# Kernel tuning notes

Hardware: AMD Instinct MI355X
Metric: run time of the kernel (lower is better)

## Reference

```python
import jax, jax.numpy as jnp
import numpy as np

NUM_EMBEDDINGS = 1024
EMBEDDING_DIM = 256
COMMITMENT_COST = 0.25


def setup_inputs() -> dict:
    key = jax.random.key(0)
    k1, k2 = jax.random.split(key)
    z_e = jax.random.normal(k1, (32, 256, 32, 32), dtype=jnp.float32)
    # nn.init.uniform_(weight, -1/K, 1/K)
    bound = 1.0 / NUM_EMBEDDINGS
    weight = jax.random.uniform(k2, (NUM_EMBEDDINGS, EMBEDDING_DIM), dtype=jnp.float32,
                                minval=-bound, maxval=bound)
    return {"z_e": z_e, "weight": weight}


def reference(z_e, weight):
    B, C, H, W = z_e.shape
    sg = jax.lax.stop_gradient
    # (B, H, W, C) -> (N, C)
    flat = jnp.transpose(z_e, (0, 2, 3, 1)).reshape(-1, C)
    # squared L2 distances to each codebook vector: (N, K)
    dist = (jnp.sum(flat * flat, axis=1, keepdims=True)
            - 2.0 * flat @ weight.T
            + jnp.sum(weight * weight, axis=1))
    indices = jnp.argmin(dist, axis=1)  # (N,)
    # codebook lookup (equivalent to one-hot @ weight)
    quantized = weight[indices].reshape(B, H, W, C)
    quantized = jnp.transpose(quantized, (0, 3, 1, 2))  # (B, C, H, W)
    e_latent = jnp.mean((sg(quantized) - z_e) ** 2)
    q_latent = jnp.mean((quantized - sg(z_e)) ** 2)
    loss = q_latent + COMMITMENT_COST * e_latent
    # straight-through estimator
    quantized_st = z_e + sg(quantized - z_e)
    # codebook usage perplexity: avg_probs = mean of one-hot encodings
    n = flat.shape[0]
    counts = jax.ops.segment_sum(jnp.ones((n,), dtype=z_e.dtype), indices,
                                 num_segments=NUM_EMBEDDINGS)
    avg_probs = counts / n
    perplexity = jnp.exp(-jnp.sum(avg_probs * jnp.log(avg_probs + 1e-10)))
    return (quantized_st, loss, perplexity)
```

## Files before the change

kernel.cpp:

```cpp
#include <hip/hip_runtime.h>
#include <float.h>
#include <math.h>
#include <stdint.h>


#define NB   32
#define NC   256
#define NHW  1024
#define NK   1024
#define NELEM (NB*NC*NHW)

typedef __attribute__((ext_vector_type(8))) short bf16x8;
typedef __attribute__((ext_vector_type(4))) float f32x4;

__device__ __forceinline__ unsigned short f2bf(float f) {
    unsigned u = __float_as_uint(f);
    u += 0x7FFFu + ((u >> 16) & 1u);
    return (unsigned short)(u >> 16);
}

__global__ __launch_bounds__(256) void vq_prep(const float* __restrict__ w,
                                               unsigned short* __restrict__ cb,
                                               float* __restrict__ wsq,
                                               unsigned int* __restrict__ counts,
                                               float* __restrict__ loss_sum) {
    __shared__ float swsq[4][16];
    const int t   = blockIdx.x;
    const int tid = threadIdx.x;
    float sq = 0.f;
#pragma unroll
    for (int rep = 0; rep < 2; ++rep) {
        const int p = tid + rep * 256;
        const int cc = p >> 6, l = p & 63;
        const int n = l & 15, quad = l >> 4;
        const float* src = w + (t * 16 + n) * NC + cc * 32 + quad * 8;
        const float4 f0 = *(const float4*)src;
        const float4 f1 = *(const float4*)(src + 4);
        union { unsigned short u[8]; uint4 v; } pk;
        pk.u[0] = f2bf(-2.f * f0.x); pk.u[1] = f2bf(-2.f * f0.y);
        pk.u[2] = f2bf(-2.f * f0.z); pk.u[3] = f2bf(-2.f * f0.w);
        pk.u[4] = f2bf(-2.f * f1.x); pk.u[5] = f2bf(-2.f * f1.y);
        pk.u[6] = f2bf(-2.f * f1.z); pk.u[7] = f2bf(-2.f * f1.w);
        *(uint4*)(cb + (size_t)t * 4096 + cc * 512 + l * 8) = pk.v;
        sq = fmaf(f0.x, f0.x, sq); sq = fmaf(f0.y, f0.y, sq);
        sq = fmaf(f0.z, f0.z, sq); sq = fmaf(f0.w, f0.w, sq);
        sq = fmaf(f1.x, f1.x, sq); sq = fmaf(f1.y, f1.y, sq);
        sq = fmaf(f1.z, f1.z, sq); sq = fmaf(f1.w, f1.w, sq);
    }
    sq += __shfl_xor(sq, 16, 64);
    sq += __shfl_xor(sq, 32, 64);
    const int wv = tid >> 6, lane = tid & 63;
    if (lane < 16) swsq[wv][lane] = sq;
    __syncthreads();
    if (tid < 16)
        wsq[t * 16 + tid] = swsq[0][tid] + swsq[1][tid] + swsq[2][tid] + swsq[3][tid];
    if (t == 0) {
        for (int i = tid; i < NK; i += 256) counts[i] = 0u;
        if (tid == 0) loss_sum[0] = 0.f;
    }
}

__global__ __launch_bounds__(256, 2) void vq_main3(const float* __restrict__ z,
                                                   const float* __restrict__ w,
                                                   const float* __restrict__ wsq,
                                                   const unsigned short* __restrict__ cb,
                                                   unsigned int* __restrict__ counts,
                                                   float* __restrict__ loss_sum,
                                                   float* __restrict__ out) {
    __shared__ float sval[4][64];
    __shared__ int   sidx[4][64];
    __shared__ int   fidx[64];
    __shared__ float lred[4];

    const int tid  = threadIdx.x;
    const int wv   = tid >> 6;
    const int lane = tid & 63;
    const int n    = lane & 15;
    const int quad = lane >> 4;
    const int bid  = blockIdx.x;
    const int b    = bid >> 4;
    const int hw0  = (bid & 15) << 6;

    const float* zb = z + (size_t)b * (NC * NHW);

    bf16x8 bfr[4][8];
#pragma unroll
    for (int nt = 0; nt < 4; ++nt) {
#pragma unroll
        for (int cc = 0; cc < 8; ++cc) {
            const float* zp = zb + (size_t)(cc * 32 + quad * 8) * NHW + hw0 + nt * 16 + n;
            union { unsigned short u[8]; bf16x8 v; } pk;
#pragma unroll
            for (int j = 0; j < 8; ++j) pk.u[j] = f2bf(zp[(size_t)j * NHW]);
            bfr[nt][cc] = pk.v;
        }
    }

    float bv[4] = {FLT_MAX, FLT_MAX, FLT_MAX, FLT_MAX};
    int   bi[4] = {0, 0, 0, 0};
    const unsigned short* ap0 = cb + (size_t)(wv * 16) * 4096 + lane * 8;

    for (int mt = 0; mt < 16; ++mt) {
        const int kt = wv * 256 + mt * 16;
        const unsigned short* ap = ap0 + (size_t)mt * 4096;
        const f32x4 w4 = *(const f32x4*)(wsq + kt + quad * 4);
        f32x4 acc[4];
#pragma unroll
        for (int nt = 0; nt < 4; ++nt) acc[nt] = w4;
#pragma unroll
        for (int cc = 0; cc < 8; ++cc) {
            const bf16x8 af = *(const bf16x8*)(ap + cc * 512);
            acc[0] = __builtin_amdgcn_mfma_f32_16x16x32_bf16(af, bfr[0][cc], acc[0], 0, 0, 0);
            acc[1] = __builtin_amdgcn_mfma_f32_16x16x32_bf16(af, bfr[1][cc], acc[1], 0, 0, 0);
            acc[2] = __builtin_amdgcn_mfma_f32_16x16x32_bf16(af, bfr[2][cc], acc[2], 0, 0, 0);
            acc[3] = __builtin_amdgcn_mfma_f32_16x16x32_bf16(af, bfr[3][cc], acc[3], 0, 0, 0);
        }
#pragma unroll
        for (int nt = 0; nt < 4; ++nt) {
#pragma unroll
            for (int r = 0; r < 4; ++r) {
                const float v = acc[nt][r];
                if (v < bv[nt]) { bv[nt] = v; bi[nt] = kt + quad * 4 + r; }
            }
        }
    }

#pragma unroll
    for (int nt = 0; nt < 4; ++nt) {
#pragma unroll
        for (int off = 16; off <= 32; off <<= 1) {
            const float ov = __shfl_xor(bv[nt], off, 64);
            const int   ok = __shfl_xor(bi[nt], off, 64);
            if (ov < bv[nt] || (ov == bv[nt] && ok < bi[nt])) { bv[nt] = ov; bi[nt] = ok; }
        }
    }
    if (lane < 16) {
#pragma unroll
        for (int nt = 0; nt < 4; ++nt) {
            sval[wv][nt * 16 + lane] = bv[nt];
            sidx[wv][nt * 16 + lane] = bi[nt];
        }
    }
    __syncthreads();

    if (tid < 64) {
        float bestv = sval[0][tid];
        int   besti = sidx[0][tid];
#pragma unroll
        for (int q = 1; q < 4; ++q) {
            const float v = sval[q][tid];
            const int   k = sidx[q][tid];
            if (v < bestv || (v == bestv && k < besti)) { bestv = v; besti = k; }
        }
        fidx[tid] = besti;
        atomicAdd(&counts[besti], 1u);
    }
    __syncthreads();

    float lsum = 0.f;
    const int hwl = tid & 63;
    const int cg  = tid >> 6;
    const int myk = fidx[hwl];
    const float* wr  = w + myk * NC;
    const float* zp2 = zb + hw0 + hwl;
    float*       op  = out + (size_t)b * (NC * NHW) + hw0 + hwl;
#pragma unroll 4
    for (int p = 0; p < 16; ++p) {
        const int c0 = cg * 64 + p * 4;
        const float4 q4 = *(const float4*)(wr + c0);
        const float qa[4] = {q4.x, q4.y, q4.z, q4.w};
#pragma unroll
        for (int u = 0; u < 4; ++u) {
            const int c = c0 + u;
            const float zv = zp2[(size_t)c * NHW];
            const float d = qa[u] - zv;
            lsum = fmaf(d, d, lsum);
            op[(size_t)c * NHW] = qa[u];
        }
    }
#pragma unroll
    for (int off = 32; off; off >>= 1) lsum += __shfl_down(lsum, off, 64);
    if (lane == 0) lred[wv] = lsum;
    __syncthreads();
    if (tid == 0)
        atomicAdd(loss_sum, lred[0] + lred[1] + lred[2] + lred[3]);
}

__global__ __launch_bounds__(256) void vq_final(const unsigned int* __restrict__ counts,
                                                const float* __restrict__ loss_sum,
                                                float* __restrict__ out) {
    __shared__ float red[4];
    const int tid = threadIdx.x;
    float s = 0.f;
#pragma unroll
    for (int p = 0; p < 4; ++p) {
        const float pr = (float)counts[tid + p * 256] * (1.f / 32768.f);
        s = fmaf(pr, logf(pr + 1e-10f), s);
    }
#pragma unroll
    for (int off = 32; off; off >>= 1) s += __shfl_down(s, off, 64);
    if ((tid & 63) == 0) red[tid >> 6] = s;
    __syncthreads();
    if (tid == 0) {
        const float tot = red[0] + red[1] + red[2] + red[3];
        out[NELEM]     = loss_sum[0] * (1.25f / (float)NELEM);
        out[NELEM + 1] = expf(-tot);
    }
}

extern "C" void kernel_launch(void* const* d_in, const int* in_sizes, int n_in,
                              void* d_out, int out_size, void* d_ws, size_t ws_size,
                              hipStream_t stream) {
    const float* z = (const float*)d_in[0];
    const float* w = (const float*)d_in[1];
    float* out = (float*)d_out;

    float*          wsq      = (float*)d_ws;
    unsigned int*   counts   = (unsigned int*)((char*)d_ws + 4096);
    float*          loss_sum = (float*)((char*)d_ws + 8192);
    unsigned short* cbfrag   = (unsigned short*)((char*)d_ws + 16384);

    vq_prep <<<64,  256, 0, stream>>>(w, cbfrag, wsq, counts, loss_sum);
    vq_main3<<<512, 256, 0, stream>>>(z, w, wsq, cbfrag, counts, loss_sum, out);
    vq_final<<<1,   256, 0, stream>>>(counts, loss_sum, out);
}
```

Baseline: 123.2 us.

## Fuse final reduction into main kernel via last-block counter; vectorize epilogue

Removes the separate finalization kernel launch. The last block to finish, found with an atomic done-counter after a threadfence, computes the perplexity and loss outputs. The gather and output epilogue is also re-mapped so each thread handles 4 consecutive spatial positions per channel, using float4 loads and stores of z and out, while the codebook values become scalar gathers. This saves a launch and its gap and widens memory accesses, at the cost of an atomic counter and strided codebook reads.

```diff
diff --git a/kernel.cpp b/kernel.cpp
--- a/kernel.cpp
+++ b/kernel.cpp
@@ -23,7 +23,8 @@
                                                unsigned short* __restrict__ cb,
                                                float* __restrict__ wsq,
                                                unsigned int* __restrict__ counts,
-                                               float* __restrict__ loss_sum) {
+                                               float* __restrict__ loss_sum,
+                                               unsigned int* __restrict__ done) {
     __shared__ float swsq[4][16];
     const int t   = blockIdx.x;
     const int tid = threadIdx.x;
@@ -56,21 +57,23 @@
         wsq[t * 16 + tid] = swsq[0][tid] + swsq[1][tid] + swsq[2][tid] + swsq[3][tid];
     if (t == 0) {
         for (int i = tid; i < NK; i += 256) counts[i] = 0u;
-        if (tid == 0) loss_sum[0] = 0.f;
-    }
-}
-
-__global__ __launch_bounds__(256, 2) void vq_main3(const float* __restrict__ z,
+        if (tid == 0) { loss_sum[0] = 0.f; done[0] = 0u; }
+    }
+}
+
+__global__ __launch_bounds__(256, 2) void vq_main6(const float* __restrict__ z,
                                                    const float* __restrict__ w,
                                                    const float* __restrict__ wsq,
                                                    const unsigned short* __restrict__ cb,
                                                    unsigned int* __restrict__ counts,
                                                    float* __restrict__ loss_sum,
+                                                   unsigned int* __restrict__ done,
                                                    float* __restrict__ out) {
     __shared__ float sval[4][64];
     __shared__ int   sidx[4][64];
     __shared__ int   fidx[64];
     __shared__ float lred[4];
+    __shared__ int   amlast;
 
     const int tid  = threadIdx.x;
     const int wv   = tid >> 6;
@@ -158,24 +161,29 @@
     __syncthreads();
 
     float lsum = 0.f;
-    const int hwl = tid & 63;
-    const int cg  = tid >> 6;
-    const int myk = fidx[hwl];
-    const float* wr  = w + myk * NC;
-    const float* zp2 = zb + hw0 + hwl;
-    float*       op  = out + (size_t)b * (NC * NHW) + hw0 + hwl;
+    {
+        const int l4 = (tid & 15) * 4;
+        const int cq = tid >> 4;
+        int k4[4];
+#pragma unroll
+        for (int u = 0; u < 4; ++u) k4[u] = fidx[l4 + u];
+        const float* zp2 = zb + hw0 + l4;
+        float*       op  = out + (size_t)b * (NC * NHW) + hw0 + l4;
 #pragma unroll 4
-    for (int p = 0; p < 16; ++p) {
-        const int c0 = cg * 64 + p * 4;
-        const float4 q4 = *(const float4*)(wr + c0);
-        const float qa[4] = {q4.x, q4.y, q4.z, q4.w};
-#pragma unroll
-        for (int u = 0; u < 4; ++u) {
-            const int c = c0 + u;
-            const float zv = zp2[(size_t)c * NHW];
-            const float d = qa[u] - zv;
-            lsum = fmaf(d, d, lsum);
-            op[(size_t)c * NHW] = qa[u];
+        for (int p = 0; p < 16; ++p) {
+            const int c = cq + p * 16;
+            const float4 zq = *(const float4*)(zp2 + (size_t)c * NHW);
+            float4 q;
+            q.x = w[k4[0] * NC + c];
+            q.y = w[k4[1] * NC + c];
+            q.z = w[k4[2] * NC + c];
+            q.w = w[k4[3] * NC + c];
+            float d;
+            d = q.x - zq.x; lsum = fmaf(d, d, lsum);
+            d = q.y - zq.y; lsum = fmaf(d, d, lsum);
+            d = q.z - zq.z; lsum = fmaf(d, d, lsum);
+            d = q.w - zq.w; lsum = fmaf(d, d, lsum);
+            *(float4*)(op + (size_t)c * NHW) = q;
         }
     }
 #pragma unroll
@@ -184,27 +192,31 @@
     __syncthreads();
     if (tid == 0)
         atomicAdd(loss_sum, lred[0] + lred[1] + lred[2] + lred[3]);
-}
-
-__global__ __launch_bounds__(256) void vq_final(const unsigned int* __restrict__ counts,
-                                                const float* __restrict__ loss_sum,
-                                                float* __restrict__ out) {
-    __shared__ float red[4];
-    const int tid = threadIdx.x;
-    float s = 0.f;
-#pragma unroll
-    for (int p = 0; p < 4; ++p) {
-        const float pr = (float)counts[tid + p * 256] * (1.f / 32768.f);
-        s = fmaf(pr, logf(pr + 1e-10f), s);
-    }
-#pragma unroll
-    for (int off = 32; off; off >>= 1) s += __shfl_down(s, off, 64);
-    if ((tid & 63) == 0) red[tid >> 6] = s;
-    __syncthreads();
+
     if (tid == 0) {
-        const float tot = red[0] + red[1] + red[2] + red[3];
-        out[NELEM]     = loss_sum[0] * (1.25f / (float)NELEM);
-        out[NELEM + 1] = expf(-tot);
+        __threadfence();
+        amlast = (atomicAdd(done, 1u) == (unsigned)(gridDim.x - 1)) ? 1 : 0;
+    }
+    __syncthreads();
+    if (amlast) {
+        float s = 0.f;
+#pragma unroll
+        for (int p = 0; p < 4; ++p) {
+            const unsigned cnt = atomicAdd(&counts[tid + p * 256], 0u);
+            const float pr = (float)cnt * (1.f / 32768.f);
+            s = fmaf(pr, logf(pr + 1e-10f), s);
+        }
+#pragma unroll
+        for (int off = 32; off; off >>= 1) s += __shfl_down(s, off, 64);
+        __syncthreads();
+        if (lane == 0) lred[wv] = s;
+        __syncthreads();
+        if (tid == 0) {
+            const float tot = lred[0] + lred[1] + lred[2] + lred[3];
+            const float lv  = atomicAdd(loss_sum, 0.f);
+            out[NELEM]     = lv * (1.25f / (float)NELEM);
+            out[NELEM + 1] = expf(-tot);
+        }
     }
 }
 
@@ -218,9 +230,9 @@
     float*          wsq      = (float*)d_ws;
     unsigned int*   counts   = (unsigned int*)((char*)d_ws + 4096);
     float*          loss_sum = (float*)((char*)d_ws + 8192);
+    unsigned int*   done     = (unsigned int*)((char*)d_ws + 8196);
     unsigned short* cbfrag   = (unsigned short*)((char*)d_ws + 16384);
 
-    vq_prep <<<64,  256, 0, stream>>>(w, cbfrag, wsq, counts, loss_sum);
-    vq_main3<<<512, 256, 0, stream>>>(z, w, wsq, cbfrag, counts, loss_sum, out);
-    vq_final<<<1,   256, 0, stream>>>(counts, loss_sum, out);
-}
+    vq_prep <<<64,  256, 0, stream>>>(w, cbfrag, wsq, counts, loss_sum, done);
+    vq_main6<<<512, 256, 0, stream>>>(z, w, wsq, cbfrag, counts, loss_sum, done, out);
+}
```

Measured after the change: 142.7 us. 15.8% more time.

## Split distance/argmin and gather-scatter into separate kernels via global index buffer

Applied to the files above, without the earlier changes.

The fused main kernel is split in two. One kernel does the MFMA distance and argmin and writes the winning indices to a global workspace buffer. A new scatter kernel with a different grid then reads 4 indices per thread, loads z with float4, gathers codebook values and writes the output with float4 stores. The aim is to let the memory-bound gather/scatter phase run with more parallelism and vectorized, coalesced access instead of serialized per-block tails. The cost is an extra launch, plus a round trip of the index buffer and a second read of z.

```diff
diff --git a/kernel.cpp b/kernel.cpp
--- a/kernel.cpp
+++ b/kernel.cpp
@@ -60,17 +60,13 @@
     }
 }
 
-__global__ __launch_bounds__(256, 2) void vq_main3(const float* __restrict__ z,
-                                                   const float* __restrict__ w,
-                                                   const float* __restrict__ wsq,
-                                                   const unsigned short* __restrict__ cb,
-                                                   unsigned int* __restrict__ counts,
-                                                   float* __restrict__ loss_sum,
-                                                   float* __restrict__ out) {
+__global__ __launch_bounds__(256, 2) void vq_dist(const float* __restrict__ z,
+                                                  const float* __restrict__ wsq,
+                                                  const unsigned short* __restrict__ cb,
+                                                  unsigned int* __restrict__ counts,
+                                                  int* __restrict__ gfidx) {
     __shared__ float sval[4][64];
     __shared__ int   sidx[4][64];
-    __shared__ int   fidx[64];
-    __shared__ float lred[4];
 
     const int tid  = threadIdx.x;
     const int wv   = tid >> 6;
@@ -152,34 +148,47 @@
             const int   k = sidx[q][tid];
             if (v < bestv || (v == bestv && k < besti)) { bestv = v; besti = k; }
         }
-        fidx[tid] = besti;
+        gfidx[b * NHW + hw0 + tid] = besti;
         atomicAdd(&counts[besti], 1u);
     }
-    __syncthreads();
+}
+
+__global__ __launch_bounds__(256, 4) void vq_scatter(const float* __restrict__ z,
+                                                     const float* __restrict__ w,
+                                                     const int* __restrict__ gfidx,
+                                                     float* __restrict__ loss_sum,
+                                                     float* __restrict__ out) {
+    __shared__ float lred[4];
+    const int tid = threadIdx.x;
+    const int bid = blockIdx.x;
+    const int b   = bid >> 5;
+    const int c0  = (bid & 31) << 3;
+    const int hw4 = tid << 2;
+
+    const int4 k4 = *(const int4*)(gfidx + b * NHW + hw4);
+    const float* zb = z   + (size_t)b * (NC * NHW);
+    float*       ob = out + (size_t)b * (NC * NHW);
 
     float lsum = 0.f;
-    const int hwl = tid & 63;
-    const int cg  = tid >> 6;
-    const int myk = fidx[hwl];
-    const float* wr  = w + myk * NC;
-    const float* zp2 = zb + hw0 + hwl;
-    float*       op  = out + (size_t)b * (NC * NHW) + hw0 + hwl;
-#pragma unroll 4
-    for (int p = 0; p < 16; ++p) {
-        const int c0 = cg * 64 + p * 4;
-        const float4 q4 = *(const float4*)(wr + c0);
-        const float qa[4] = {q4.x, q4.y, q4.z, q4.w};
-#pragma unroll
-        for (int u = 0; u < 4; ++u) {
-            const int c = c0 + u;
-            const float zv = zp2[(size_t)c * NHW];
-            const float d = qa[u] - zv;
-            lsum = fmaf(d, d, lsum);
-            op[(size_t)c * NHW] = qa[u];
-        }
+#pragma unroll
+    for (int i = 0; i < 8; ++i) {
+        const int c = c0 + i;
+        const float4 zq = *(const float4*)(zb + (size_t)c * NHW + hw4);
+        float4 q;
+        q.x = w[k4.x * NC + c];
+        q.y = w[k4.y * NC + c];
+        q.z = w[k4.z * NC + c];
+        q.w = w[k4.w * NC + c];
+        float d;
+        d = q.x - zq.x; lsum = fmaf(d, d, lsum);
+        d = q.y - zq.y; lsum = fmaf(d, d, lsum);
+        d = q.z - zq.z; lsum = fmaf(d, d, lsum);
+        d = q.w - zq.w; lsum = fmaf(d, d, lsum);
+        *(float4*)(ob + (size_t)c * NHW + hw4) = q;
     }
 #pragma unroll
     for (int off = 32; off; off >>= 1) lsum += __shfl_down(lsum, off, 64);
+    const int lane = tid & 63, wv = tid >> 6;
     if (lane == 0) lred[wv] = lsum;
     __syncthreads();
     if (tid == 0)
@@ -219,8 +228,10 @@
     unsigned int*   counts   = (unsigned int*)((char*)d_ws + 4096);
     float*          loss_sum = (float*)((char*)d_ws + 8192);
     unsigned short* cbfrag   = (unsigned short*)((char*)d_ws + 16384);
-
-    vq_prep <<<64,  256, 0, stream>>>(w, cbfrag, wsq, counts, loss_sum);
-    vq_main3<<<512, 256, 0, stream>>>(z, w, wsq, cbfrag, counts, loss_sum, out);
-    vq_final<<<1,   256, 0, stream>>>(counts, loss_sum, out);
-}
+    int*            gfidx    = (int*)((char*)d_ws + 540672);
+
+    vq_prep   <<<64,   256, 0, stream>>>(w, cbfrag, wsq, counts, loss_sum);
+    vq_dist   <<<512,  256, 0, stream>>>(z, wsq, cbfrag, counts, gfidx);
+    vq_scatter<<<1024, 256, 0, stream>>>(z, w, gfidx, loss_sum, out);
+    vq_final  <<<1,    256, 0, stream>>>(counts, loss_sum, out);
+}
```

Result: slower. 138.2 us (+12.2%).

## Prefetch codebook fragments into registers and fold final reduction into main kernel

Applied to the files above, without the earlier changes.

The main kernel now software-pipelines the codebook A-fragment loads with a triple-buffered register prefetch two tiles ahead, so global loads overlap the MFMA work. The separate finalization kernel is removed: the last block to finish, found through an atomic done counter with a threadfence, computes perplexity and loss. This saves one kernel launch and hides load latency, but raises register pressure (an extra 24 bf16x8 vectors per lane alongside the 32 already held) under launch_bounds(256,2), which could cause spills.

```diff
diff --git a/kernel.cpp b/kernel.cpp
--- a/kernel.cpp
+++ b/kernel.cpp
@@ -23,7 +23,8 @@
                                                unsigned short* __restrict__ cb,
                                                float* __restrict__ wsq,
                                                unsigned int* __restrict__ counts,
-                                               float* __restrict__ loss_sum) {
+                                               float* __restrict__ loss_sum,
+                                               unsigned int* __restrict__ done) {
     __shared__ float swsq[4][16];
     const int t   = blockIdx.x;
     const int tid = threadIdx.x;
@@ -56,21 +57,23 @@
         wsq[t * 16 + tid] = swsq[0][tid] + swsq[1][tid] + swsq[2][tid] + swsq[3][tid];
     if (t == 0) {
         for (int i = tid; i < NK; i += 256) counts[i] = 0u;
-        if (tid == 0) loss_sum[0] = 0.f;
-    }
-}
-
-__global__ __launch_bounds__(256, 2) void vq_main3(const float* __restrict__ z,
+        if (tid == 0) { loss_sum[0] = 0.f; done[0] = 0u; }
+    }
+}
+
+__global__ __launch_bounds__(256, 2) void vq_main8(const float* __restrict__ z,
                                                    const float* __restrict__ w,
                                                    const float* __restrict__ wsq,
                                                    const unsigned short* __restrict__ cb,
                                                    unsigned int* __restrict__ counts,
                                                    float* __restrict__ loss_sum,
+                                                   unsigned int* __restrict__ done,
                                                    float* __restrict__ out) {
     __shared__ float sval[4][64];
     __shared__ int   sidx[4][64];
     __shared__ int   fidx[64];
     __shared__ float lred[4];
+    __shared__ int   amlast;
 
     const int tid  = threadIdx.x;
     const int wv   = tid >> 6;
@@ -82,6 +85,13 @@
     const int hw0  = (bid & 15) << 6;
 
     const float* zb = z + (size_t)b * (NC * NHW);
+    const unsigned short* ap0 = cb + (size_t)(wv * 16) * 4096 + lane * 8;
+
+    bf16x8 pf[3][8];
+#pragma unroll
+    for (int cc = 0; cc < 8; ++cc) pf[0][cc] = *(const bf16x8*)(ap0 + cc * 512);
+#pragma unroll
+    for (int cc = 0; cc < 8; ++cc) pf[1][cc] = *(const bf16x8*)(ap0 + 4096 + cc * 512);
 
     bf16x8 bfr[4][8];
 #pragma unroll
@@ -98,18 +108,23 @@
 
     float bv[4] = {FLT_MAX, FLT_MAX, FLT_MAX, FLT_MAX};
     int   bi[4] = {0, 0, 0, 0};
-    const unsigned short* ap0 = cb + (size_t)(wv * 16) * 4096 + lane * 8;
-
+
+#pragma unroll 16
     for (int mt = 0; mt < 16; ++mt) {
+        if (mt + 2 < 16) {
+            const unsigned short* apn = ap0 + (size_t)(mt + 2) * 4096;
+#pragma unroll
+            for (int cc = 0; cc < 8; ++cc)
+                pf[(mt + 2) % 3][cc] = *(const bf16x8*)(apn + cc * 512);
+        }
         const int kt = wv * 256 + mt * 16;
-        const unsigned short* ap = ap0 + (size_t)mt * 4096;
         const f32x4 w4 = *(const f32x4*)(wsq + kt + quad * 4);
         f32x4 acc[4];
 #pragma unroll
         for (int nt = 0; nt < 4; ++nt) acc[nt] = w4;
 #pragma unroll
         for (int cc = 0; cc < 8; ++cc) {
-            const bf16x8 af = *(const bf16x8*)(ap + cc * 512);
+            const bf16x8 af = pf[mt % 3][cc];
             acc[0] = __builtin_amdgcn_mfma_f32_16x16x32_bf16(af, bfr[0][cc], acc[0], 0, 0, 0);
             acc[1] = __builtin_amdgcn_mfma_f32_16x16x32_bf16(af, bfr[1][cc], acc[1], 0, 0, 0);
             acc[2] = __builtin_amdgcn_mfma_f32_16x16x32_bf16(af, bfr[2][cc], acc[2], 0, 0, 0);
@@ -184,27 +199,31 @@
     __syncthreads();
     if (tid == 0)
         atomicAdd(loss_sum, lred[0] + lred[1] + lred[2] + lred[3]);
-}
-
-__global__ __launch_bounds__(256) void vq_final(const unsigned int* __restrict__ counts,
-                                                const float* __restrict__ loss_sum,
-                                                float* __restrict__ out) {
-    __shared__ float red[4];
-    const int tid = threadIdx.x;
-    float s = 0.f;
-#pragma unroll
-    for (int p = 0; p < 4; ++p) {
-        const float pr = (float)counts[tid + p * 256] * (1.f / 32768.f);
-        s = fmaf(pr, logf(pr + 1e-10f), s);
-    }
-#pragma unroll
-    for (int off = 32; off; off >>= 1) s += __shfl_down(s, off, 64);
-    if ((tid & 63) == 0) red[tid >> 6] = s;
-    __syncthreads();
+
     if (tid == 0) {
-        const float tot = red[0] + red[1] + red[2] + red[3];
-        out[NELEM]     = loss_sum[0] * (1.25f / (float)NELEM);
-        out[NELEM + 1] = expf(-tot);
+        __threadfence();
+        amlast = (atomicAdd(done, 1u) == (unsigned)(gridDim.x - 1)) ? 1 : 0;
+    }
+    __syncthreads();
+    if (amlast) {
+        float s = 0.f;
+#pragma unroll
+        for (int p = 0; p < 4; ++p) {
+            const unsigned cnt = atomicAdd(&counts[tid + p * 256], 0u);
+            const float pr = (float)cnt * (1.f / 32768.f);
+            s = fmaf(pr, logf(pr + 1e-10f), s);
+        }
+#pragma unroll
+        for (int off = 32; off; off >>= 1) s += __shfl_down(s, off, 64);
+        __syncthreads();
+        if (lane == 0) lred[wv] = s;
+        __syncthreads();
+        if (tid == 0) {
+            const float tot = lred[0] + lred[1] + lred[2] + lred[3];
+            const float lv  = atomicAdd(loss_sum, 0.f);
+            out[NELEM]     = lv * (1.25f / (float)NELEM);
+            out[NELEM + 1] = expf(-tot);
+        }
     }
 }
 
@@ -218,9 +237,9 @@
     float*          wsq      = (float*)d_ws;
     unsigned int*   counts   = (unsigned int*)((char*)d_ws + 4096);
     float*          loss_sum = (float*)((char*)d_ws + 8192);
+    unsigned int*   done     = (unsigned int*)((char*)d_ws + 8196);
     unsigned short* cbfrag   = (unsigned short*)((char*)d_ws + 16384);
 
-    vq_prep <<<64,  256, 0, stream>>>(w, cbfrag, wsq, counts, loss_sum);
-    vq_main3<<<512, 256, 0, stream>>>(z, w, wsq, cbfrag, counts, loss_sum, out);
-    vq_final<<<1,   256, 0, stream>>>(counts, loss_sum, out);
-}
+    vq_prep <<<64,  256, 0, stream>>>(w, cbfrag, wsq, counts, loss_sum, done);
+    vq_main8<<<512, 256, 0, stream>>>(z, w, wsq, cbfrag, counts, loss_sum, done, out);
+}
```

Measured after the change: 173.2 us. 40.5% more time.
